# Kernel tuning notes

Hardware: AMD Instinct MI355X
Metric: run time of the kernel (lower is better)

Reference implementation:

```python
import jax, jax.numpy as jnp
import numpy as np

B, S, L = 64, 512, 768


def setup_inputs() -> dict:
    key = jax.random.key(0)
    k1, k2 = jax.random.split(key)
    x = jax.random.normal(k1, (B, S, L), dtype=jnp.float32)
    # matches torch uniform_(-0.1, 0.1) init for the probe matrix b
    b = jax.random.uniform(k2, (L, L), minval=-0.1, maxval=0.1, dtype=jnp.float32)
    return {"x": x, "b": b}


def reference(x, b):
    # Original: z[b,i,j,h] = x_i - x_j; h = einsum('gh,bijh', b, z); dist = sum_g h^2
    # Identity: ||b @ (x_i - x_j)||^2 = ||p_i||^2 + ||p_j||^2 - 2 p_i . p_j,  p = x @ b^T
    p = jnp.einsum('gh,bsh->bsg', b, x)          # [B, S, L] projected points
    sq = jnp.sum(p * p, axis=-1)                 # [B, S]  squared norms
    gram = jnp.einsum('bsg,btg->bst', p, p)      # [B, S, S] inner products
    return sq[:, :, None] + sq[:, None, :] - 2.0 * gram  # [B, S, S]
```

## Files before the change

### kernel.cpp

```cpp
#include <hip/hip_runtime.h>
#include <hip/hip_bf16.h>


using bf16x8 = __attribute__((ext_vector_type(8))) __bf16;
using f32x4  = __attribute__((ext_vector_type(4))) float;
using fl4    = __attribute__((ext_vector_type(4))) float;
using u16x4  = __attribute__((ext_vector_type(4))) unsigned short;

#define NB 64
#define NS 512
#define NL 768

__device__ __forceinline__ unsigned short f2bf(float f) {
  unsigned u = __builtin_bit_cast(unsigned, f);
  u += 0x7FFFu + ((u >> 16) & 1u);
  return (unsigned short)(u >> 16);
}

__device__ __forceinline__ void gload_lds16(const void* g, void* l) {
  __builtin_amdgcn_global_load_lds(
      (const __attribute__((address_space(1))) void*)g,
      (__attribute__((address_space(3))) void*)l, 16, 0, 0);
}

#define MEMFENCE asm volatile("" ::: "memory")

__global__ __launch_bounds__(256) void k_cvt_b(const float* __restrict__ b,
                                               unsigned short* __restrict__ bb) {
  const long t = (long)blockIdx.x * 256 + threadIdx.x;
  fl4 v = *(const fl4*)(b + t * 4);
  u16x4 o;
#pragma unroll
  for (int j = 0; j < 4; ++j) o[j] = f2bf(v[j]);
  *(u16x4*)(bb + t * 4) = o;
}

__global__ __launch_bounds__(256) void k_cvt_x(const float* __restrict__ x,
                                               unsigned short* __restrict__ xb,
                                               float* __restrict__ sq) {
  if (blockIdx.x < 128) sq[blockIdx.x * 256 + threadIdx.x] = 0.f;
  const long n4 = (long)NB * NS * NL / 4;
  const long stride = (long)gridDim.x * 256;
  for (long i = (long)blockIdx.x * 256 + threadIdx.x; i < n4; i += stride) {
    fl4 v = *(const fl4*)(x + i * 4);
    u16x4 o;
#pragma unroll
    for (int j = 0; j < 4; ++j) o[j] = f2bf(v[j]);
    *(u16x4*)(xb + i * 4) = o;
  }
}

__global__ __launch_bounds__(256) void k_projb(
    const unsigned short* __restrict__ xb,
    const unsigned short* __restrict__ bb,
    unsigned short* __restrict__ p,
    float* __restrict__ sq) {
  __shared__ __align__(16) unsigned short smA[3][128 * 32];
  __shared__ __align__(16) unsigned short smB[3][128 * 32];
  const int tid = threadIdx.x;
  const int w = tid >> 6, l = tid & 63;
  const int wg = ((blockIdx.x & 7) * 192) + (blockIdx.x >> 3);
  const int nt = wg % 6, mt = wg / 6;
  const long m0 = (long)mt * 128, n0 = (long)nt * 128;
  const int wr = (w >> 1) * 64, wc = (w & 1) * 64;

  const int srow = tid >> 2;
  const int scol = ((tid & 3) ^ ((srow >> 1) & 3)) * 8;
  const unsigned short* gA = xb + (m0 + srow) * (long)NL + scol;
  const unsigned short* gB = bb + (n0 + srow) * (long)NL + scol;

  const int qh = l >> 4, lr = l & 15;
  const int aoff = (wr + lr) * 64 + ((qh ^ ((lr >> 1) & 3)) << 4);
  const int boff = (wc + lr) * 64 + ((qh ^ ((lr >> 1) & 3)) << 4);

  f32x4 acc[4][4] = {};

#define STAGEP(k0, buf)                                                      \
  {                                                                          \
    char* da_ = (char*)&smA[buf][0] + w * 1024;                              \
    char* db_ = (char*)&smB[buf][0] + w * 1024;                              \
    gload_lds16(gA + (k0), da_);                                             \
    gload_lds16(gA + (k0) + 64 * NL, da_ + 4096);                            \
    gload_lds16(gB + (k0), db_);                                             \
    gload_lds16(gB + (k0) + 64 * NL, db_ + 4096);                            \
  }
#define COMPUTEP(buf)                                                        \
  {                                                                          \
    const char* A_ = (const char*)&smA[buf][0];                              \
    const char* B_ = (const char*)&smB[buf][0];                              \
    bf16x8 fa[4], fb[4];                                                     \
    _Pragma("unroll")                                                        \
    for (int m = 0; m < 4; ++m)                                              \
      fa[m] = *(const bf16x8*)(A_ + aoff + m * 1024);                        \
    _Pragma("unroll")                                                        \
    for (int n = 0; n < 4; ++n)                                              \
      fb[n] = *(const bf16x8*)(B_ + boff + n * 1024);                        \
    _Pragma("unroll")                                                        \
    for (int m = 0; m < 4; ++m)                                              \
      _Pragma("unroll")                                                      \
      for (int n = 0; n < 4; ++n)                                            \
        acc[m][n] = __builtin_amdgcn_mfma_f32_16x16x32_bf16(fa[m], fb[n],    \
                                                            acc[m][n], 0, 0, 0); \
  }

  STAGEP(0, 0)
  STAGEP(32, 1)
  int cur = 0, nxt2 = 2;
#pragma unroll 1
  for (int kt = 0; kt < 23; ++kt) {
    asm volatile("s_waitcnt vmcnt(4)" ::: "memory");
    __builtin_amdgcn_s_barrier();
    MEMFENCE;
    if (kt < 22) STAGEP((kt + 2) * 32, nxt2)
    COMPUTEP(cur)
    cur = (cur == 2) ? 0 : cur + 1;
    nxt2 = (nxt2 == 2) ? 0 : nxt2 + 1;
  }
  asm volatile("s_waitcnt vmcnt(0)" ::: "memory");
  __builtin_amdgcn_s_barrier();
  MEMFENCE;
  COMPUTEP(cur)
#undef STAGEP
#undef COMPUTEP

#pragma unroll
  for (int m = 0; m < 4; ++m) {
    const long rbase = m0 + wr + m * 16 + qh * 4;
#pragma unroll
    for (int r = 0; r < 4; ++r) {
      const long row = rbase + r;
      float s = 0.f;
#pragma unroll
      for (int n = 0; n < 4; ++n) {
        const unsigned short us = f2bf(acc[m][n][r]);
        p[row * NL + (n0 + wc + n * 16 + lr)] = us;
        const float f = __builtin_bit_cast(float, ((unsigned)us) << 16);
        s += f * f;
      }
      s += __shfl_xor(s, 1, 64);
      s += __shfl_xor(s, 2, 64);
      s += __shfl_xor(s, 4, 64);
      s += __shfl_xor(s, 8, 64);
      if (lr == 0) atomicAdd(sq + row, s);
    }
  }
}

__global__ __launch_bounds__(256) void k_gram(const unsigned short* __restrict__ p,
                                              const float* __restrict__ sq,
                                              float* __restrict__ out) {
  __shared__ __align__(16) unsigned short smA[3][128 * 32];
  __shared__ __align__(16) unsigned short smB[3][128 * 32];
  const int tid = threadIdx.x;
  const int w = tid >> 6, l = tid & 63;
  const int wg = ((blockIdx.x & 7) * 128) + (blockIdx.x >> 3);
  const int batch = wg >> 4, tile = wg & 15;
  const int mt = tile >> 2, nt = tile & 3;
  const unsigned short* pb = p + (long)batch * NS * NL;
  const long m0 = (long)mt * 128, n0 = (long)nt * 128;
  const int wr = (w >> 1) * 64, wc = (w & 1) * 64;

  const int srow = tid >> 2;
  const int scol = ((tid & 3) ^ ((srow >> 1) & 3)) * 8;
  const unsigned short* gA = pb + (m0 + srow) * (long)NL + scol;
  const unsigned short* gB = pb + (n0 + srow) * (long)NL + scol;

  const int qh = l >> 4, lr = l & 15;
  const int aoff = (wr + lr) * 64 + ((qh ^ ((lr >> 1) & 3)) << 4);
  const int boff = (wc + lr) * 64 + ((qh ^ ((lr >> 1) & 3)) << 4);

  f32x4 acc[4][4] = {};

#define STAGE2(k0, buf)                                                      \
  {                                                                          \
    char* da_ = (char*)&smA[buf][0] + w * 1024;                              \
    char* db_ = (char*)&smB[buf][0] + w * 1024;                              \
    gload_lds16(gA + (k0), da_);                                             \
    gload_lds16(gA + (k0) + 64 * NL, da_ + 4096);                            \
    gload_lds16(gB + (k0), db_);                                             \
    gload_lds16(gB + (k0) + 64 * NL, db_ + 4096);                            \
  }
#define COMPUTE2(buf)                                                        \
  {                                                                          \
    const char* A_ = (const char*)&smA[buf][0];                              \
    const char* B_ = (const char*)&smB[buf][0];                              \
    bf16x8 fa[4], fb[4];                                                     \
    _Pragma("unroll")                                                        \
    for (int m = 0; m < 4; ++m)                                              \
      fa[m] = *(const bf16x8*)(A_ + aoff + m * 1024);                        \
    _Pragma("unroll")                                                        \
    for (int n = 0; n < 4; ++n)                                              \
      fb[n] = *(const bf16x8*)(B_ + boff + n * 1024);                        \
    _Pragma("unroll")                                                        \
    for (int m = 0; m < 4; ++m)                                              \
      _Pragma("unroll")                                                      \
      for (int n = 0; n < 4; ++n)                                            \
        acc[m][n] = __builtin_amdgcn_mfma_f32_16x16x32_bf16(fa[m], fb[n],    \
                                                            acc[m][n], 0, 0, 0); \
  }

  STAGE2(0, 0)
  STAGE2(32, 1)
  int cur = 0, nxt2 = 2;
#pragma unroll 1
  for (int kt = 0; kt < 23; ++kt) {
    asm volatile("s_waitcnt vmcnt(4)" ::: "memory");
    __builtin_amdgcn_s_barrier();
    MEMFENCE;
    if (kt < 22) STAGE2((kt + 2) * 32, nxt2)
    COMPUTE2(cur)
    cur = (cur == 2) ? 0 : cur + 1;
    nxt2 = (nxt2 == 2) ? 0 : nxt2 + 1;
  }
  asm volatile("s_waitcnt vmcnt(0)" ::: "memory");
  __builtin_amdgcn_s_barrier();
  MEMFENCE;
  COMPUTE2(cur)
#undef STAGE2
#undef COMPUTE2

  const float* sqb = sq + batch * NS;
  float* outb = out + (long)batch * NS * NS;
  float sqc[4];
#pragma unroll
  for (int n = 0; n < 4; ++n) sqc[n] = sqb[n0 + wc + n * 16 + lr];
#pragma unroll
  for (int m = 0; m < 4; ++m) {
#pragma unroll
    for (int r = 0; r < 4; ++r) {
      const long row = m0 + wr + m * 16 + qh * 4 + r;
      const float sr = sqb[row];
#pragma unroll
      for (int n = 0; n < 4; ++n) {
        const long col = n0 + wc + n * 16 + lr;
        outb[row * NS + col] = sr + sqc[n] - 2.0f * acc[m][n][r];
      }
    }
  }
}

extern "C" void kernel_launch(void* const* d_in, const int* in_sizes, int n_in,
                              void* d_out, int out_size, void* d_ws, size_t ws_size,
                              hipStream_t stream) {
  (void)in_sizes; (void)n_in; (void)out_size; (void)ws_size;
  const float* x = (const float*)d_in[0];
  const float* b = (const float*)d_in[1];
  float* out = (float*)d_out;
  char* ws = (char*)d_ws;
  unsigned short* bb = (unsigned short*)ws;
  float* sq          = (float*)(ws + 1179648);
  unsigned short* p  = (unsigned short*)(ws + 1310720);
  unsigned short* xb = (unsigned short*)(ws + 51642368);

  k_cvt_b<<<576, 256, 0, stream>>>(b, bb);
  k_cvt_x<<<2048, 256, 0, stream>>>(x, xb, sq);
  k_projb<<<1536, 256, 0, stream>>>(xb, bb, p, sq);
  k_gram <<<1024, 256, 0, stream>>>(p, sq, out);
}
```

Measured before the change: 136.0 us.

## Enlarge projection tile to 128x256 with 512 threads; replace atomics with partial-sum reduction

The projection GEMM now uses 512-thread blocks computing 128x256 output tiles, so each A tile is reused across twice as many columns and global traffic for x drops. B staging is double-buffered while A keeps three buffers, with an adjusted wait count. Row squared-norm atomics are replaced by per-column-group partial sums written to a workspace, which a new small kernel reduces. The x conversion kernel is also widened to 8 elements per thread. This adds a kernel launch and changes occupancy and LDS usage.

```diff
diff --git a/kernel.cpp b/kernel.cpp
--- a/kernel.cpp
+++ b/kernel.cpp
@@ -6,10 +6,12 @@
 using f32x4  = __attribute__((ext_vector_type(4))) float;
 using fl4    = __attribute__((ext_vector_type(4))) float;
 using u16x4  = __attribute__((ext_vector_type(4))) unsigned short;
+using u16x8  = __attribute__((ext_vector_type(8))) unsigned short;
 
 #define NB 64
 #define NS 512
 #define NL 768
+#define NM (NB * NS)
 
 __device__ __forceinline__ unsigned short f2bf(float f) {
   unsigned u = __builtin_bit_cast(unsigned, f);
@@ -36,58 +38,62 @@
 }
 
 __global__ __launch_bounds__(256) void k_cvt_x(const float* __restrict__ x,
-                                               unsigned short* __restrict__ xb,
-                                               float* __restrict__ sq) {
-  if (blockIdx.x < 128) sq[blockIdx.x * 256 + threadIdx.x] = 0.f;
-  const long n4 = (long)NB * NS * NL / 4;
+                                               unsigned short* __restrict__ xb) {
+  const long n8 = (long)NM * NL / 8;
   const long stride = (long)gridDim.x * 256;
-  for (long i = (long)blockIdx.x * 256 + threadIdx.x; i < n4; i += stride) {
-    fl4 v = *(const fl4*)(x + i * 4);
-    u16x4 o;
-#pragma unroll
-    for (int j = 0; j < 4; ++j) o[j] = f2bf(v[j]);
-    *(u16x4*)(xb + i * 4) = o;
-  }
-}
-
-__global__ __launch_bounds__(256) void k_projb(
+  for (long i = (long)blockIdx.x * 256 + threadIdx.x; i < n8; i += stride) {
+    fl4 v0 = *(const fl4*)(x + i * 8);
+    fl4 v1 = *(const fl4*)(x + i * 8 + 4);
+    u16x8 o;
+#pragma unroll
+    for (int j = 0; j < 4; ++j) { o[j] = f2bf(v0[j]); o[j + 4] = f2bf(v1[j]); }
+    *(u16x8*)(xb + i * 8) = o;
+  }
+}
+
+__global__ __launch_bounds__(512) void k_projb(
     const unsigned short* __restrict__ xb,
     const unsigned short* __restrict__ bb,
     unsigned short* __restrict__ p,
-    float* __restrict__ sq) {
+    float* __restrict__ spart) {
   __shared__ __align__(16) unsigned short smA[3][128 * 32];
-  __shared__ __align__(16) unsigned short smB[3][128 * 32];
+  __shared__ __align__(16) unsigned short smB[2][256 * 32];
   const int tid = threadIdx.x;
   const int w = tid >> 6, l = tid & 63;
-  const int wg = ((blockIdx.x & 7) * 192) + (blockIdx.x >> 3);
-  const int nt = wg % 6, mt = wg / 6;
-  const long m0 = (long)mt * 128, n0 = (long)nt * 128;
-  const int wr = (w >> 1) * 64, wc = (w & 1) * 64;
-
-  const int srow = tid >> 2;
-  const int scol = ((tid & 3) ^ ((srow >> 1) & 3)) * 8;
-  const unsigned short* gA = xb + (m0 + srow) * (long)NL + scol;
-  const unsigned short* gB = bb + (n0 + srow) * (long)NL + scol;
+  const int wg = ((blockIdx.x & 7) * 96) + (blockIdx.x >> 3);
+  const int nt = wg % 3, mt = wg / 3;
+  const long m0 = (long)mt * 128, n0 = (long)nt * 256;
+  const int wr = (w >> 2) * 64, wc = (w & 3) * 64;
+
+  const int arow = (w << 4) + (l >> 2);
+  const int acol = ((l & 3) ^ ((arow >> 1) & 3)) * 8;
+  const unsigned short* gA = xb + (m0 + arow) * (long)NL + acol;
+  const int brow = (w << 5) + (l >> 2);
+  const int bcol = ((l & 3) ^ ((brow >> 1) & 3)) * 8;
+  const unsigned short* gB = bb + (n0 + brow) * (long)NL + bcol;
 
   const int qh = l >> 4, lr = l & 15;
-  const int aoff = (wr + lr) * 64 + ((qh ^ ((lr >> 1) & 3)) << 4);
-  const int boff = (wc + lr) * 64 + ((qh ^ ((lr >> 1) & 3)) << 4);
+  const int swz = ((qh ^ ((lr >> 1) & 3)) << 4);
+  const int aoff = (wr + lr) * 64 + swz;
+  const int boff = (wc + lr) * 64 + swz;
 
   f32x4 acc[4][4] = {};
 
-#define STAGEP(k0, buf)                                                      \
+#define STAGE_B(k0, buf)                                                     \
+  {                                                                          \
+    char* db_ = (char*)&smB[buf][0] + w * 2048;                              \
+    gload_lds16(gB + (k0), db_);                                             \
+    gload_lds16(gB + (k0) + 16 * NL, db_ + 1024);                            \
+  }
+#define STAGE_A(k0, buf)                                                     \
   {                                                                          \
     char* da_ = (char*)&smA[buf][0] + w * 1024;                              \
-    char* db_ = (char*)&smB[buf][0] + w * 1024;                              \
     gload_lds16(gA + (k0), da_);                                             \
-    gload_lds16(gA + (k0) + 64 * NL, da_ + 4096);                            \
-    gload_lds16(gB + (k0), db_);                                             \
-    gload_lds16(gB + (k0) + 64 * NL, db_ + 4096);                            \
-  }
-#define COMPUTEP(buf)                                                        \
-  {                                                                          \
-    const char* A_ = (const char*)&smA[buf][0];                              \
-    const char* B_ = (const char*)&smB[buf][0];                              \
+  }
+#define COMPUTEP(bA, bB)                                                     \
+  {                                                                          \
+    const char* A_ = (const char*)&smA[bA][0];                               \
+    const char* B_ = (const char*)&smB[bB][0];                               \
     bf16x8 fa[4], fb[4];                                                     \
     _Pragma("unroll")                                                        \
     for (int m = 0; m < 4; ++m)                                              \
@@ -103,24 +109,29 @@
                                                             acc[m][n], 0, 0, 0); \
   }
 
-  STAGEP(0, 0)
-  STAGEP(32, 1)
-  int cur = 0, nxt2 = 2;
+  STAGE_B(0, 0)
+  STAGE_A(0, 0)
+  STAGE_A(32, 1)
+  int bufA = 0;
 #pragma unroll 1
   for (int kt = 0; kt < 23; ++kt) {
-    asm volatile("s_waitcnt vmcnt(4)" ::: "memory");
+    asm volatile("s_waitcnt vmcnt(1)" ::: "memory");
     __builtin_amdgcn_s_barrier();
     MEMFENCE;
-    if (kt < 22) STAGEP((kt + 2) * 32, nxt2)
-    COMPUTEP(cur)
-    cur = (cur == 2) ? 0 : cur + 1;
-    nxt2 = (nxt2 == 2) ? 0 : nxt2 + 1;
+    STAGE_B((kt + 1) * 32, (kt + 1) & 1)
+    if (kt < 22) {
+      const int bA2 = (bufA >= 1) ? bufA - 1 : bufA + 2;
+      STAGE_A((kt + 2) * 32, bA2)
+    }
+    COMPUTEP(bufA, kt & 1)
+    bufA = (bufA == 2) ? 0 : bufA + 1;
   }
   asm volatile("s_waitcnt vmcnt(0)" ::: "memory");
   __builtin_amdgcn_s_barrier();
   MEMFENCE;
-  COMPUTEP(cur)
-#undef STAGEP
+  COMPUTEP(bufA, 1)
+#undef STAGE_B
+#undef STAGE_A
 #undef COMPUTEP
 
 #pragma unroll
@@ -141,9 +152,18 @@
       s += __shfl_xor(s, 2, 64);
       s += __shfl_xor(s, 4, 64);
       s += __shfl_xor(s, 8, 64);
-      if (lr == 0) atomicAdd(sq + row, s);
+      if (lr == 0) spart[(long)(nt * 4 + (w & 3)) * NM + row] = s;
     }
   }
+}
+
+__global__ __launch_bounds__(256) void k_sqsum(const float* __restrict__ spart,
+                                               float* __restrict__ sq) {
+  const int row = blockIdx.x * 256 + threadIdx.x;
+  float s = 0.f;
+#pragma unroll
+  for (int j = 0; j < 12; ++j) s += spart[(long)j * NM + row];
+  sq[row] = s;
 }
 
 __global__ __launch_bounds__(256) void k_gram(const unsigned short* __restrict__ p,
@@ -249,11 +269,13 @@
   char* ws = (char*)d_ws;
   unsigned short* bb = (unsigned short*)ws;
   float* sq          = (float*)(ws + 1179648);
-  unsigned short* p  = (unsigned short*)(ws + 1310720);
-  unsigned short* xb = (unsigned short*)(ws + 51642368);
+  float* spart       = (float*)(ws + 1310720);
+  unsigned short* p  = (unsigned short*)(ws + 2883584);
+  unsigned short* xb = (unsigned short*)(ws + 53215232);
 
   k_cvt_b<<<576, 256, 0, stream>>>(b, bb);
-  k_cvt_x<<<2048, 256, 0, stream>>>(x, xb, sq);
-  k_projb<<<1536, 256, 0, stream>>>(xb, bb, p, sq);
+  k_cvt_x<<<2048, 256, 0, stream>>>(x, xb);
+  k_projb<<<768, 512, 0, stream>>>(xb, bb, p, spart);
+  k_sqsum<<<128, 256, 0, stream>>>(spart, sq);
   k_gram <<<1024, 256, 0, stream>>>(p, sq, out);
 }
```

New measurement: 132.0 us. 3.0% less time.
